# Performance work log

Measured on AMD Instinct MI355X. Metric: run time of the kernel, lower is better.

The kernel has to match this reference:

```python
import jax, jax.numpy as jnp
import numpy as np

B, L, D, H, BASE = 4, 2048, 768, 12, 10000
HD = D // H  # 64


def _rope_tables(seq_len, head_dim, base, dtype):
    # inv_freq over even indices, freqs duplicated for rotate-half layout
    inv_freq = 1.0 / (base ** (jnp.arange(0, head_dim, 2, dtype=jnp.float32) / head_dim))
    pos = jnp.arange(seq_len, dtype=jnp.float32)
    freqs = pos[:, None] * inv_freq[None, :]          # [L, HD/2]
    emb = jnp.concatenate([freqs, freqs], axis=-1)    # [L, HD]
    return jnp.cos(emb).astype(dtype), jnp.sin(emb).astype(dtype)


def _rotate_half(x):
    h = x.shape[-1] // 2
    return jnp.concatenate([-x[..., h:], x[..., :h]], axis=-1)


def setup_inputs() -> dict:
    key = jax.random.key(0)
    k0, k1, k2 = jax.random.split(key, 3)
    input_embeddings = jax.random.normal(k0, (B, L, D), dtype=jnp.float32)
    padding_mask = jnp.zeros((B, L), dtype=bool)  # True = ignore (padding)
    W_qkv = jax.random.normal(k1, (D, 3 * D), dtype=jnp.float32) * 0.02
    b_qkv = jnp.zeros((3 * D,), dtype=jnp.float32)
    W_out = jax.random.normal(k2, (D, D), dtype=jnp.float32) * 0.02
    b_out = jnp.zeros((D,), dtype=jnp.float32)
    return {"input_embeddings": input_embeddings, "padding_mask": padding_mask,
            "W_qkv": W_qkv, "b_qkv": b_qkv, "W_out": W_out, "b_out": b_out}


def reference(input_embeddings, padding_mask, W_qkv, b_qkv, W_out, b_out):
    x = input_embeddings
    dtype = x.dtype
    neg_big = -jnp.finfo(dtype).max

    qkv = x @ W_qkv + b_qkv                       # [B, L, 3D]
    q, k, v = jnp.split(qkv, 3, axis=-1)
    # b l (h d) -> b h l d
    to_heads = lambda t: t.reshape(B, L, H, HD).transpose(0, 2, 1, 3)
    q, k, v = to_heads(q), to_heads(k), to_heads(v)

    # RoPE (start_pos = 0, no kv cache)
    cos, sin = _rope_tables(L, HD, BASE, dtype)   # [L, HD]
    cos, sin = cos[None, None], sin[None, None]
    q = q * cos + _rotate_half(q) * sin
    k = k * cos + _rotate_half(k) * sin

    sims = jnp.einsum('bhqd,bhkd->bhqk', q, k) / jnp.sqrt(jnp.asarray(HD, dtype))
    # padding mask: True -> -inf on key axis
    sims = jnp.where(padding_mask[:, None, None, :], neg_big, sims)
    # causal mask triu(1)
    causal = jnp.triu(jnp.ones((L, L), dtype=bool), 1)
    sims = jnp.where(causal[None, None], neg_big, sims)

    attn_probs = jax.nn.softmax(sims, axis=-1)    # [B, H, L, L]
    attn_out = jnp.einsum('bhqk,bhkd->bhqd', attn_probs, v)
    attn_out = attn_out.transpose(0, 2, 1, 3).reshape(B, L, D)
    output = attn_out @ W_out + b_out             # [B, L, D]
    return output
```

## Files before the change

kernel.cpp:

```cpp
#include <hip/hip_runtime.h>
#include <hip/hip_bf16.h>


#define B_  4
#define L_  2048
#define D_  768
#define H_  12
#define HD_ 64
#define THREED (3 * D_)
#define LOG2E 1.4426950408889634f

typedef __attribute__((ext_vector_type(8))) short short8;
typedef __attribute__((ext_vector_type(4))) float f32x4;
typedef __attribute__((ext_vector_type(16))) float f32x16;
typedef __attribute__((ext_vector_type(4))) __bf16 bf16x4;
typedef __attribute__((ext_vector_type(2))) __bf16 bf16x2;

__device__ __forceinline__ unsigned short f2bf(float f) {
    union { float f; unsigned u; } a; a.f = f;
    unsigned r = a.u + 0x7FFFu + ((a.u >> 16) & 1u);
    return (unsigned short)(r >> 16);
}

__device__ __forceinline__ unsigned pk2bf(float a, float b) {
    union { bf16x2 v; unsigned u; } t;
    t.v[0] = (__bf16)a; t.v[1] = (__bf16)b;
    return t.u;
}

__device__ __forceinline__ void async_ld16(const void* g, void* l) {
    __builtin_amdgcn_global_load_lds(
        (const __attribute__((address_space(1))) void*)g,
        (__attribute__((address_space(3))) void*)l,
        16, 0, 0);
}

#define PREP_CONV   3072
#define PREP_TQKV   1728
#define PREP_TOUT   576
#define PREP_ROPE   256
__global__ __launch_bounds__(256) void prep(const float* __restrict__ x,
                                            unsigned short* __restrict__ xb,
                                            const float* __restrict__ Wqkv,
                                            unsigned short* __restrict__ WqkvT,
                                            const float* __restrict__ Wout,
                                            unsigned short* __restrict__ WoutT,
                                            float2* __restrict__ cs) {
    __shared__ float tl[32][33];
    const int blk = blockIdx.x;
    const int tid = threadIdx.x;
    if (blk < PREP_CONV) {
        const int i = blk * 256 + tid;
        float4 f0 = ((const float4*)x)[i * 2];
        float4 f1 = ((const float4*)x)[i * 2 + 1];
        short8 u;
        u[0] = f2bf(f0.x); u[1] = f2bf(f0.y); u[2] = f2bf(f0.z); u[3] = f2bf(f0.w);
        u[4] = f2bf(f1.x); u[5] = f2bf(f1.y); u[6] = f2bf(f1.z); u[7] = f2bf(f1.w);
        ((short8*)xb)[i] = u;
    } else if (blk < PREP_CONV + PREP_TQKV + PREP_TOUT) {
        const bool qkv = blk < PREP_CONV + PREP_TQKV;
        const int idx = qkv ? blk - PREP_CONV : blk - PREP_CONV - PREP_TQKV;
        const int nb = qkv ? (THREED / 32) : (D_ / 32);
        const int N = qkv ? THREED : D_;
        const float* in = qkv ? Wqkv : Wout;
        unsigned short* out = qkv ? WqkvT : WoutT;
        const int n0 = (idx % nb) * 32, k0 = (idx / nb) * 32;
        const int tx = tid & 31, ty = tid >> 5;
        #pragma unroll
        for (int i = 0; i < 4; ++i)
            tl[ty + 8 * i][tx] = in[(size_t)(k0 + ty + 8 * i) * N + n0 + tx];
        __syncthreads();
        #pragma unroll
        for (int i = 0; i < 4; ++i)
            out[(size_t)(n0 + ty + 8 * i) * D_ + k0 + tx] = f2bf(tl[tx][ty + 8 * i]);
    } else {
        const int i = (blk - PREP_CONV - PREP_TQKV - PREP_TOUT) * 256 + tid;
        const int pos = i >> 5, t = i & 31;
        float invf = powf(10000.0f, -(float)t / 32.0f);
        float s, c;
        sincosf((float)pos * invf, &s, &c);
        cs[i] = make_float2(c, s);
    }
}

__global__ __launch_bounds__(512) void qkv_gemm(const unsigned short* __restrict__ A,
                                                const unsigned short* __restrict__ BT,
                                                const float* __restrict__ bias,
                                                unsigned short* __restrict__ C,
                                                const float2* __restrict__ cs,
                                                unsigned short* __restrict__ VtOut) {
    __shared__ __align__(16) unsigned short As[2][256 * 32];
    __shared__ __align__(16) unsigned short Bs[2][128 * 32];
    const int tid = threadIdx.x;
    const int w = tid >> 6, lane = tid & 63;
    const int quad = lane >> 4, lr = lane & 15;
    const int wm = w >> 1, wn = w & 1;
    const int m0 = blockIdx.x * 256, n0 = blockIdx.y * 128;

    int arow[2], acol[2];
    #pragma unroll
    for (int i = 0; i < 2; ++i) {
        const int s = i * 512 + tid;
        arow[i] = s >> 2;
        acol[i] = ((s & 3) ^ ((arow[i] >> 1) & 3)) * 8;
    }
    const int brow = tid >> 2;
    const int bcol = ((tid & 3) ^ ((brow >> 1) & 3)) * 8;

    f32x4 acc[4][4];
    #pragma unroll
    for (int i = 0; i < 4; ++i)
        #pragma unroll
        for (int j = 0; j < 4; ++j)
            acc[i][j] = (f32x4){0.f, 0.f, 0.f, 0.f};

    #pragma unroll
    for (int i = 0; i < 2; ++i)
        async_ld16(A + (size_t)(m0 + arow[i]) * D_ + acol[i],
                   &As[0][(size_t)(i * 512 + w * 64) * 8]);
    async_ld16(BT + (size_t)(n0 + brow) * D_ + bcol, &Bs[0][(size_t)(w * 64) * 8]);
    __syncthreads();

    const int iters = D_ / 32;
    for (int it = 0; it < iters; ++it) {
        const int cur = it & 1;
        if (it + 1 < iters) {
            const int k1 = (it + 1) * 32;
            #pragma unroll
            for (int i = 0; i < 2; ++i)
                async_ld16(A + (size_t)(m0 + arow[i]) * D_ + k1 + acol[i],
                           &As[cur ^ 1][(size_t)(i * 512 + w * 64) * 8]);
            async_ld16(BT + (size_t)(n0 + brow) * D_ + k1 + bcol,
                       &Bs[cur ^ 1][(size_t)(w * 64) * 8]);
        }
        short8 af[4], bfr[4];
        #pragma unroll
        for (int mt = 0; mt < 4; ++mt) {
            const int ra = wm * 64 + mt * 16 + lr;
            af[mt] = *(const short8*)&As[cur][(size_t)(ra * 4 + (quad ^ ((ra >> 1) & 3))) * 8];
        }
        #pragma unroll
        for (int nt = 0; nt < 4; ++nt) {
            const int rb = wn * 64 + nt * 16 + lr;
            bfr[nt] = *(const short8*)&Bs[cur][(size_t)(rb * 4 + (quad ^ ((rb >> 1) & 3))) * 8];
        }
        #pragma unroll
        for (int mt = 0; mt < 4; ++mt)
            #pragma unroll
            for (int nt = 0; nt < 4; ++nt)
                acc[mt][nt] = __builtin_amdgcn_mfma_f32_16x16x32_bf16(
                    af[mt], bfr[nt], acc[mt][nt], 0, 0, 0);
        __syncthreads();
    }

    float bv[4];
    #pragma unroll
    for (int nt = 0; nt < 4; ++nt)
        bv[nt] = bias[n0 + wn * 64 + nt * 16 + lr];

    const int hd0 = n0 + wn * 64;
    const int hb = hd0 >> 6;
    if (hb < 24) {
        const float scl = (hb < 12) ? 0.125f * LOG2E : 1.0f;
        #pragma unroll
        for (int mt = 0; mt < 4; ++mt)
            #pragma unroll
            for (int reg = 0; reg < 4; ++reg) {
                const int row = m0 + wm * 64 + mt * 16 + quad * 4 + reg;
                const float2* csr = cs + (size_t)(row & (L_ - 1)) * 32;
                #pragma unroll
                for (int nt2 = 0; nt2 < 2; ++nt2) {
                    const int t = nt2 * 16 + lr;
                    float2 p = csr[t];
                    const float cx = p.x * scl, sx = p.y * scl;
                    const float x1 = acc[mt][nt2][reg] + bv[nt2];
                    const float x2 = acc[mt][nt2 + 2][reg] + bv[nt2 + 2];
                    unsigned pk = (unsigned)f2bf(x1 * cx - x2 * sx)
                                | ((unsigned)f2bf(x2 * cx + x1 * sx) << 16);
                    *(unsigned*)&C[(size_t)row * THREED + hd0 + 2 * t] = pk;
                }
            }
    } else {
        const int h = hb - 24;
        #pragma unroll
        for (int mt = 0; mt < 4; ++mt) {
            const int l = m0 + wm * 64 + mt * 16 + quad * 4;
            const int b = l >> 11, lloc = l & (L_ - 1);
            #pragma unroll
            for (int nt = 0; nt < 4; ++nt) {
                const int d = nt * 16 + lr;
                ushort4 u;
                u.x = f2bf(acc[mt][nt][0] + bv[nt]);
                u.y = f2bf(acc[mt][nt][1] + bv[nt]);
                u.z = f2bf(acc[mt][nt][2] + bv[nt]);
                u.w = f2bf(acc[mt][nt][3] + bv[nt]);
                *(ushort4*)&VtOut[((size_t)((b * H_ + h) * HD_ + d)) * L_ + lloc] = u;
            }
        }
    }
}

__global__ __launch_bounds__(256) void out_gemm(const unsigned short* __restrict__ A, int lda,
                                                const unsigned short* __restrict__ BT,
                                                const float* __restrict__ bias,
                                                float* __restrict__ C,
                                                int M, int N, int K) {
    __shared__ __align__(16) unsigned short As[2][128 * 32];
    __shared__ __align__(16) unsigned short Bs[2][128 * 32];
    const int tid = threadIdx.x;
    const int w = tid >> 6, lane = tid & 63;
    const int quad = lane >> 4, lr = lane & 15;
    const int wm = w & 1, wn = w >> 1;
    const int m0 = blockIdx.x * 128, n0 = blockIdx.y * 128;

    int grow[2], gcol[2], ldst[2];
    #pragma unroll
    for (int i = 0; i < 2; ++i) {
        const int slot = i * 256 + tid;
        grow[i] = slot >> 2;
        gcol[i] = ((slot & 3) ^ ((grow[i] >> 1) & 3)) * 8;
        ldst[i] = (i * 256 + (tid & ~63)) * 8;
    }

    f32x4 acc[4][4];
    #pragma unroll
    for (int i = 0; i < 4; ++i)
        #pragma unroll
        for (int j = 0; j < 4; ++j)
            acc[i][j] = (f32x4){0.f, 0.f, 0.f, 0.f};

    #pragma unroll
    for (int i = 0; i < 2; ++i) {
        async_ld16(BT + (size_t)(n0 + grow[i]) * K + gcol[i], &Bs[0][ldst[i]]);
        async_ld16(A + (size_t)(m0 + grow[i]) * lda + gcol[i], &As[0][ldst[i]]);
    }
    __syncthreads();

    const int iters = K >> 5;
    for (int it = 0; it < iters; ++it) {
        const int cur = it & 1;
        if (it + 1 < iters) {
            const int k1 = (it + 1) << 5;
            #pragma unroll
            for (int i = 0; i < 2; ++i) {
                async_ld16(BT + (size_t)(n0 + grow[i]) * K + k1 + gcol[i], &Bs[cur ^ 1][ldst[i]]);
                async_ld16(A + (size_t)(m0 + grow[i]) * lda + k1 + gcol[i], &As[cur ^ 1][ldst[i]]);
            }
        }
        short8 af[4], bfr[4];
        #pragma unroll
        for (int mt = 0; mt < 4; ++mt) {
            const int ra = wm * 64 + mt * 16 + lr;
            af[mt] = *(const short8*)&As[cur][(size_t)(ra * 4 + (quad ^ ((ra >> 1) & 3))) * 8];
        }
        #pragma unroll
        for (int nt = 0; nt < 4; ++nt) {
            const int rb = wn * 64 + nt * 16 + lr;
            bfr[nt] = *(const short8*)&Bs[cur][(size_t)(rb * 4 + (quad ^ ((rb >> 1) & 3))) * 8];
        }
        #pragma unroll
        for (int mt = 0; mt < 4; ++mt)
            #pragma unroll
            for (int nt = 0; nt < 4; ++nt)
                acc[mt][nt] = __builtin_amdgcn_mfma_f32_16x16x32_bf16(
                    af[mt], bfr[nt], acc[mt][nt], 0, 0, 0);
        __syncthreads();
    }

    float bv[4];
    #pragma unroll
    for (int nt = 0; nt < 4; ++nt)
        bv[nt] = bias[n0 + wn * 64 + nt * 16 + lr];
    #pragma unroll
    for (int mt = 0; mt < 4; ++mt)
        #pragma unroll
        for (int nt = 0; nt < 4; ++nt) {
            const int col = n0 + wn * 64 + nt * 16 + lr;
            #pragma unroll
            for (int reg = 0; reg < 4; ++reg) {
                const int row = m0 + wm * 64 + mt * 16 + quad * 4 + reg;
                C[(size_t)row * N + col] = acc[mt][nt][reg] + bv[nt];
            }
        }
}

__global__ __launch_bounds__(256, 3) void attn_mfma(unsigned short* __restrict__ qkvb,
                                                    const unsigned short* __restrict__ Vt) {
    __shared__ __align__(16) unsigned short Ks[2][64 * 64];
    __shared__ __align__(16) unsigned short Vs[2][64 * 64];

    const int qtb = gridDim.y - 1 - blockIdx.y;
    const int bh = blockIdx.x;
    const int b = bh / H_, h = bh % H_;
    const int tid = threadIdx.x;
    const int w = tid >> 6, lane = tid & 63;
    const int lq = lane & 31, hi = lane >> 5;
    const int qw = qtb * 128 + w * 32;
    const int ktmax = 2 * qtb + 1;
    const int lim = 2 * qtb + (w >> 1);

    int sr[2], sc[2];
    #pragma unroll
    for (int i = 0; i < 2; ++i) {
        const int s = i * 256 + tid;
        sr[i] = s >> 3;
        sc[i] = ((s & 7) ^ (sr[i] & 7)) * 8;
    }
    const int wbase = tid & ~63;

    const size_t qrow = (size_t)(b * L_ + qw + lq) * THREED + h * HD_;
    short8 qf[4];
    #pragma unroll
    for (int st = 0; st < 4; ++st)
        qf[st] = *(const short8*)&qkvb[qrow + st * 16 + hi * 8];

    f32x16 o0, o1;
    #pragma unroll
    for (int i = 0; i < 16; ++i) { o0[i] = 0.f; o1[i] = 0.f; }
    float l_run = 0.f;

    #pragma unroll
    for (int i = 0; i < 2; ++i) {
        async_ld16(qkvb + ((size_t)(b * L_ + sr[i])) * THREED + D_ + h * HD_ + sc[i],
                   &Ks[0][(size_t)(i * 256 + wbase) * 8]);
        async_ld16(Vt + ((size_t)(bh * HD_ + sr[i])) * L_ + sc[i],
                   &Vs[0][(size_t)(i * 256 + wbase) * 8]);
    }
    __syncthreads();

    for (int kt = 0; kt <= ktmax; ++kt) {
        const int cur = kt & 1;
        if (kt < ktmax) {
            const size_t krow0 = (size_t)(b * L_ + (kt + 1) * 64);
            #pragma unroll
            for (int i = 0; i < 2; ++i) {
                async_ld16(qkvb + (krow0 + sr[i]) * THREED + D_ + h * HD_ + sc[i],
                           &Ks[cur ^ 1][(size_t)(i * 256 + wbase) * 8]);
                async_ld16(Vt + ((size_t)(bh * HD_ + sr[i])) * L_ + (kt + 1) * 64 + sc[i],
                           &Vs[cur ^ 1][(size_t)(i * 256 + wbase) * 8]);
            }
        }

        if (kt <= lim) {
            f32x16 s0, s1;
            #pragma unroll
            for (int i = 0; i < 16; ++i) { s0[i] = 0.f; s1[i] = 0.f; }
            #pragma unroll
            for (int st = 0; st < 4; ++st) {
                const int cg = st * 2 + hi;
                short8 ak0 = *(const short8*)&Ks[cur][(size_t)(lq * 8 + (cg ^ (lq & 7))) * 8];
                short8 ak1 = *(const short8*)&Ks[cur][(size_t)((32 + lq) * 8 + (cg ^ (lq & 7))) * 8];
                s0 = __builtin_amdgcn_mfma_f32_32x32x16_bf16(ak0, qf[st], s0, 0, 0, 0);
                s1 = __builtin_amdgcn_mfma_f32_32x32x16_bf16(ak1, qf[st], s1, 0, 0, 0);
            }

            if (kt == lim) {
                const int qloc = (w & 1) * 32 + lq;
                #pragma unroll
                for (int reg = 0; reg < 16; ++reg) {
                    const int r = (reg & 3) + 8 * (reg >> 2) + 4 * hi;
                    s0[reg] = (r > qloc) ? 0.f : exp2f(s0[reg]);
                    s1[reg] = (r + 32 > qloc) ? 0.f : exp2f(s1[reg]);
                }
            } else {
                #pragma unroll
                for (int reg = 0; reg < 16; ++reg) {
                    s0[reg] = exp2f(s0[reg]);
                    s1[reg] = exp2f(s1[reg]);
                }
            }
            float rs = 0.f;
            #pragma unroll
            for (int reg = 0; reg < 16; ++reg) rs += s0[reg] + s1[reg];
            l_run += rs;

            short8 pf[4];
            #pragma unroll
            for (int kb = 0; kb < 2; ++kb) {
                const f32x16 sv = kb ? s1 : s0;
                #pragma unroll
                for (int h2 = 0; h2 < 2; ++h2) {
                    const int rb = h2 * 8;
                    unsigned a0 = pk2bf(sv[rb + 0], sv[rb + 1]);
                    unsigned a1 = pk2bf(sv[rb + 2], sv[rb + 3]);
                    unsigned b0 = pk2bf(sv[rb + 4], sv[rb + 5]);
                    unsigned b1 = pk2bf(sv[rb + 6], sv[rb + 7]);
                    asm("v_permlane32_swap_b32 %0, %1" : "+v"(a0), "+v"(b0));
                    asm("v_permlane32_swap_b32 %0, %1" : "+v"(a1), "+v"(b1));
                    union { unsigned u[4]; short8 v; } t;
                    t.u[0] = a0; t.u[1] = a1; t.u[2] = b0; t.u[3] = b1;
                    pf[kb * 2 + h2] = t.v;
                }
            }

            #pragma unroll
            for (int t4 = 0; t4 < 4; ++t4) {
                const int cg = t4 * 2 + hi;
                short8 av0 = *(const short8*)&Vs[cur][(size_t)(lq * 8 + (cg ^ (lq & 7))) * 8];
                short8 av1 = *(const short8*)&Vs[cur][(size_t)((32 + lq) * 8 + (cg ^ (lq & 7))) * 8];
                o0 = __builtin_amdgcn_mfma_f32_32x32x16_bf16(av0, pf[t4], o0, 0, 0, 0);
                o1 = __builtin_amdgcn_mfma_f32_32x32x16_bf16(av1, pf[t4], o1, 0, 0, 0);
            }
        }
        __syncthreads();
    }

    const float lt = l_run + __shfl_xor(l_run, 32);
    const float inv = 1.0f / lt;
    unsigned short* dst = qkvb + qrow;
    #pragma unroll
    for (int db = 0; db < 2; ++db) {
        const f32x16 ov = db ? o1 : o0;
        #pragma unroll
        for (int g = 0; g < 4; ++g) {
            const int d0 = db * 32 + g * 8 + 4 * hi;
            ushort4 u;
            u.x = f2bf(ov[g * 4 + 0] * inv);
            u.y = f2bf(ov[g * 4 + 1] * inv);
            u.z = f2bf(ov[g * 4 + 2] * inv);
            u.w = f2bf(ov[g * 4 + 3] * inv);
            *(ushort4*)&dst[d0] = u;
        }
    }
}

extern "C" void kernel_launch(void* const* d_in, const int* in_sizes, int n_in,
                              void* d_out, int out_size, void* d_ws, size_t ws_size,
                              hipStream_t stream) {
    const float* x    = (const float*)d_in[0];
    const float* Wqkv = (const float*)d_in[2];
    const float* bqkv = (const float*)d_in[3];
    const float* Wout = (const float*)d_in[4];
    const float* bout = (const float*)d_in[5];
    float* out = (float*)d_out;

    unsigned short* qkvb  = (unsigned short*)d_ws;
    unsigned short* Vt    = qkvb + (size_t)(B_ * L_) * THREED;
    unsigned short* xb    = Vt + (size_t)(B_ * H_) * HD_ * L_;
    unsigned short* WqkvT = xb + (size_t)(B_ * L_) * D_;
    unsigned short* WoutT = WqkvT + (size_t)THREED * D_;
    float2* rope_cs = (float2*)(WoutT + (size_t)D_ * D_);

    prep<<<PREP_CONV + PREP_TQKV + PREP_TOUT + PREP_ROPE, 256, 0, stream>>>(
        x, xb, Wqkv, WqkvT, Wout, WoutT, rope_cs);
    qkv_gemm<<<dim3((B_ * L_) / 256, THREED / 128), 512, 0, stream>>>(
        xb, WqkvT, bqkv, qkvb, rope_cs, Vt);
    attn_mfma<<<dim3(B_ * H_, L_ / 128), 256, 0, stream>>>(qkvb, Vt);
    out_gemm<<<dim3((B_ * L_) / 128, D_ / 128), 256, 0, stream>>>(
        qkvb, THREED, WoutT, bout, out, B_ * L_, D_, D_);
}
```

Before: 209.7 us.

## Triple-buffer K/V tiles with single barrier per iteration and MFMA priority

Expands the K/V shared-memory staging from two to three buffers, so each loop iteration needs only one barrier. That barrier waits with a partial vmcnt, letting the next tile's async loads stay in flight while the current tile is computed. It also wraps the MFMA sections in s_setprio raises and seeds the first QK MFMA with a zero accumulator instead of zeroing registers. The extra 16KB of LDS could limit occupancy at three blocks per CU. The hand-written vmcnt count has to match the async load count exactly to stay correct.

```diff
diff --git a/kernel.cpp b/kernel.cpp
--- a/kernel.cpp
+++ b/kernel.cpp
@@ -286,8 +286,8 @@
 
 __global__ __launch_bounds__(256, 3) void attn_mfma(unsigned short* __restrict__ qkvb,
                                                     const unsigned short* __restrict__ Vt) {
-    __shared__ __align__(16) unsigned short Ks[2][64 * 64];
-    __shared__ __align__(16) unsigned short Vs[2][64 * 64];
+    __shared__ __align__(16) unsigned short Ks[3][64 * 64];
+    __shared__ __align__(16) unsigned short Vs[3][64 * 64];
 
     const int qtb = gridDim.y - 1 - blockIdx.y;
     const int bh = blockIdx.x;
@@ -314,9 +314,11 @@
     for (int st = 0; st < 4; ++st)
         qf[st] = *(const short8*)&qkvb[qrow + st * 16 + hi * 8];
 
-    f32x16 o0, o1;
-    #pragma unroll
-    for (int i = 0; i < 16; ++i) { o0[i] = 0.f; o1[i] = 0.f; }
+    f32x16 Z;
+    #pragma unroll
+    for (int i = 0; i < 16; ++i) Z[i] = 0.f;
+
+    f32x16 o0 = Z, o1 = Z;
     float l_run = 0.f;
 
     #pragma unroll
@@ -326,33 +328,42 @@
         async_ld16(Vt + ((size_t)(bh * HD_ + sr[i])) * L_ + sc[i],
                    &Vs[0][(size_t)(i * 256 + wbase) * 8]);
     }
-    __syncthreads();
-
+
+    int cur = 0, nxt = 1;
     for (int kt = 0; kt <= ktmax; ++kt) {
-        const int cur = kt & 1;
         if (kt < ktmax) {
             const size_t krow0 = (size_t)(b * L_ + (kt + 1) * 64);
             #pragma unroll
             for (int i = 0; i < 2; ++i) {
                 async_ld16(qkvb + (krow0 + sr[i]) * THREED + D_ + h * HD_ + sc[i],
-                           &Ks[cur ^ 1][(size_t)(i * 256 + wbase) * 8]);
+                           &Ks[nxt][(size_t)(i * 256 + wbase) * 8]);
                 async_ld16(Vt + ((size_t)(bh * HD_ + sr[i])) * L_ + (kt + 1) * 64 + sc[i],
-                           &Vs[cur ^ 1][(size_t)(i * 256 + wbase) * 8]);
-            }
+                           &Vs[nxt][(size_t)(i * 256 + wbase) * 8]);
+            }
+            asm volatile("s_waitcnt vmcnt(4)\n\ts_barrier" ::: "memory");
+        } else {
+            asm volatile("s_waitcnt vmcnt(0)\n\ts_barrier" ::: "memory");
         }
 
         if (kt <= lim) {
             f32x16 s0, s1;
-            #pragma unroll
-            for (int i = 0; i < 16; ++i) { s0[i] = 0.f; s1[i] = 0.f; }
-            #pragma unroll
-            for (int st = 0; st < 4; ++st) {
+            {
+                const int cg = hi;
+                short8 ak0 = *(const short8*)&Ks[cur][(size_t)(lq * 8 + (cg ^ (lq & 7))) * 8];
+                short8 ak1 = *(const short8*)&Ks[cur][(size_t)((32 + lq) * 8 + (cg ^ (lq & 7))) * 8];
+                __builtin_amdgcn_s_setprio(1);
+                s0 = __builtin_amdgcn_mfma_f32_32x32x16_bf16(ak0, qf[0], Z, 0, 0, 0);
+                s1 = __builtin_amdgcn_mfma_f32_32x32x16_bf16(ak1, qf[0], Z, 0, 0, 0);
+            }
+            #pragma unroll
+            for (int st = 1; st < 4; ++st) {
                 const int cg = st * 2 + hi;
                 short8 ak0 = *(const short8*)&Ks[cur][(size_t)(lq * 8 + (cg ^ (lq & 7))) * 8];
                 short8 ak1 = *(const short8*)&Ks[cur][(size_t)((32 + lq) * 8 + (cg ^ (lq & 7))) * 8];
                 s0 = __builtin_amdgcn_mfma_f32_32x32x16_bf16(ak0, qf[st], s0, 0, 0, 0);
                 s1 = __builtin_amdgcn_mfma_f32_32x32x16_bf16(ak1, qf[st], s1, 0, 0, 0);
             }
+            __builtin_amdgcn_s_setprio(0);
 
             if (kt == lim) {
                 const int qloc = (w & 1) * 32 + lq;
@@ -393,6 +404,7 @@
                 }
             }
 
+            __builtin_amdgcn_s_setprio(1);
             #pragma unroll
             for (int t4 = 0; t4 < 4; ++t4) {
                 const int cg = t4 * 2 + hi;
@@ -401,8 +413,10 @@
                 o0 = __builtin_amdgcn_mfma_f32_32x32x16_bf16(av0, pf[t4], o0, 0, 0, 0);
                 o1 = __builtin_amdgcn_mfma_f32_32x32x16_bf16(av1, pf[t4], o1, 0, 0, 0);
             }
-        }
-        __syncthreads();
+            __builtin_amdgcn_s_setprio(0);
+        }
+        cur = nxt;
+        nxt = (nxt + 1 == 3) ? 0 : nxt + 1;
     }
 
     const float lt = l_run + __shfl_xor(l_run, 32);
```

New measurement: 209.6 us. About the same (-0.1%).
